# Kernel tuning notes

Measured on AMD Instinct MI355X. Metric: run time of the kernel, lower is better.

The kernel has to match this reference:

```python
import jax, jax.numpy as jnp
import numpy as np

N = 100000
E = 1600000
F_IN = 256
HID = 128
N_CLS = 2


def _glorot(k, shape):
    lim = float(np.sqrt(6.0 / (shape[0] + shape[1])))
    return jax.random.uniform(k, shape, jnp.float32, -lim, lim)


def setup_inputs() -> dict:
    key = jax.random.key(0)
    ks = jax.random.split(key, 10)
    x = jax.random.normal(ks[0], (N, F_IN), jnp.float32)
    edge_index = jax.random.randint(ks[1], (2, E), 0, N, dtype=jnp.int64)
    return {
        "x": x,
        "edge_index": edge_index,
        "W1": _glorot(ks[2], (F_IN, HID)), "b1": jnp.zeros((HID,), jnp.float32),
        "W2": _glorot(ks[3], (HID, HID)), "b2": jnp.zeros((HID,), jnp.float32),
        "W3": _glorot(ks[4], (HID, HID)), "b3": jnp.zeros((HID,), jnp.float32),
        "Wc": _glorot(ks[5], (HID, N_CLS)), "bc": jnp.zeros((N_CLS,), jnp.float32),
    }


def gcn_layer(x, W, b, src, dst, n):
    """PyG GCNConv: D^-1/2 (A+I) D^-1/2 X W + b with self-loops added."""
    xw = x @ W  # [N, H]
    # degree including the self-loop (all edge weights are 1)
    deg = jax.ops.segment_sum(jnp.ones((src.shape[0],), xw.dtype), dst,
                              num_segments=n) + 1.0
    dinv = jax.lax.rsqrt(deg)  # [N]
    norm = dinv[src] * dinv[dst]  # [E]
    msg = xw[src] * norm[:, None]  # [E, H] gathered+scaled messages
    out = jax.ops.segment_sum(msg, dst, num_segments=n)
    # self-loop contribution: norm = dinv[i]*dinv[i] = 1/deg[i]
    out = out + xw * (1.0 / deg)[:, None]
    return out + b


def reference(x, edge_index, W1, b1, W2, b2, W3, b3, Wc, bc):
    src, dst = edge_index[0], edge_index[1]
    h = jax.nn.relu(gcn_layer(x, W1, b1, src, dst, N))
    h = jax.nn.relu(gcn_layer(h, W2, b2, src, dst, N))  # dropout identity (eval)
    h = jax.nn.relu(gcn_layer(h, W3, b3, src, dst, N))
    logits = h @ Wc + bc  # [N, num_classes]
    return jax.nn.log_softmax(logits, axis=1)
```

## Files before the change

kernel.cpp:

```cpp
#include <hip/hip_runtime.h>
#include <hip/hip_bf16.h>
#include <cstdint>
#include <cstddef>

#define N_NODES 100000
#define N_EDGES 1600000
#define F_IN    256
#define HID     128
#define SCAN_BLK 1024
#define N_SCAN_BLOCKS ((N_NODES + SCAN_BLK - 1) / SCAN_BLK)
#define NB       ((N_NODES + 255) >> 8)
#define F3_CHUNK 7168
#define N_CHUNKS ((N_EDGES + F3_CHUNK - 1) / F3_CHUNK)

typedef __attribute__((ext_vector_type(8))) short  bf16x8;
typedef __attribute__((ext_vector_type(4))) float  f32x4;

static __device__ inline float bf2f(unsigned short u) {
    return __uint_as_float(((unsigned int)u) << 16);
}
static __device__ inline unsigned short f2bf(float f) {
    union { __hip_bfloat16 h; unsigned short u; } c;
    c.h = __float2bfloat16(f);
    return c.u;
}
static __device__ inline float lof(unsigned int w) { return __uint_as_float(w << 16); }
static __device__ inline float hif(unsigned int w) { return __uint_as_float(w & 0xffff0000u); }


__global__ __launch_bounds__(256) void zero_int_kernel(int* __restrict__ p, int n) {
    int i = blockIdx.x * 256 + threadIdx.x;
    if (i < n) p[i] = 0;
}
__global__ __launch_bounds__(256) void zero_f_kernel(float* __restrict__ p, int n) {
    int i = blockIdx.x * 256 + threadIdx.x;
    if (i < n) p[i] = 0.f;
}


__global__ __launch_bounds__(256) void bucket_count_kernel(const int* __restrict__ dst,
                                                           int* __restrict__ bcnt, int nE) {
    __shared__ int c[NB];
    for (int i = threadIdx.x; i < NB; i += 256) c[i] = 0;
    __syncthreads();
    int base = blockIdx.x * F3_CHUNK;
    int m = min(F3_CHUNK, nE - base);
    for (int t = threadIdx.x; t < m; t += 256)
        atomicAdd(&c[dst[base + t] >> 8], 1);
    __syncthreads();
    for (int i = threadIdx.x; i < NB; i += 256)
        if (c[i]) atomicAdd(&bcnt[i], c[i]);
}


__global__ __launch_bounds__(512) void scan_bucket_kernel(const int* __restrict__ bcnt,
                                                          int* __restrict__ bbase) {
    __shared__ int s[512];
    int t = threadIdx.x;
    int v = (t < NB) ? bcnt[t] : 0;
    s[t] = v;
    __syncthreads();
    for (int off = 1; off < 512; off <<= 1) {
        int add = (t >= off) ? s[t - off] : 0;
        __syncthreads();
        s[t] += add;
        __syncthreads();
    }
    if (t < NB) bbase[t] = s[t] - v;
    if (t == 0) bbase[NB] = N_EDGES;
}


__global__ __launch_bounds__(256) void stage_kernel(const int* __restrict__ src,
                                                    const int* __restrict__ dst,
                                                    const int* __restrict__ bbase,
                                                    int* __restrict__ gfill,
                                                    int* __restrict__ stg_src,
                                                    int* __restrict__ stg_dst, int nE) {
    __shared__ int ss[F3_CHUNK];
    __shared__ int sd[F3_CHUNK];
    __shared__ int cnt[NB];
    __shared__ int bas[NB];
    int base = blockIdx.x * F3_CHUNK;
    int m = min(F3_CHUNK, nE - base);
    for (int i = threadIdx.x; i < NB; i += 256) cnt[i] = 0;
    __syncthreads();
    for (int t = threadIdx.x; t < m; t += 256) {
        int s = src[base + t];
        int d = dst[base + t];
        ss[t] = s;
        sd[t] = d;
        atomicAdd(&cnt[d >> 8], 1);
    }
    __syncthreads();
    for (int i = threadIdx.x; i < NB; i += 256) {
        int c = cnt[i];
        bas[i] = bbase[i] + (c ? atomicAdd(&gfill[i], c) : 0);
        cnt[i] = 0;
    }
    __syncthreads();
    for (int t = threadIdx.x; t < m; t += 256) {
        int d = sd[t];
        int bkt = d >> 8;
        int k = atomicAdd(&cnt[bkt], 1);
        int pos = bas[bkt] + k;
        stg_src[pos] = ss[t];
        stg_dst[pos] = d;
    }
}


__global__ __launch_bounds__(256) void bucket_deg_kernel(const int* __restrict__ stg_dst,
                                                         const int* __restrict__ bbase,
                                                         int* __restrict__ deg, int n) {
    __shared__ int c[256];
    c[threadIdx.x] = 0;
    __syncthreads();
    int b = blockIdx.x;
    int beg = bbase[b], end = bbase[b + 1];
    for (int t = beg + threadIdx.x; t < end; t += 256)
        atomicAdd(&c[stg_dst[t] & 255], 1);
    __syncthreads();
    int node = b * 256 + threadIdx.x;
    if (node < n) deg[node] = c[threadIdx.x];
}


__global__ __launch_bounds__(256) void bucket_fill_kernel(const int* __restrict__ stg_src,
                                                          const int* __restrict__ stg_dst,
                                                          const int* __restrict__ bbase,
                                                          const int* __restrict__ row_ptr,
                                                          int* __restrict__ csr_src) {
    __shared__ int c[256];
    c[threadIdx.x] = 0;
    __syncthreads();
    int b = blockIdx.x;
    int beg = bbase[b], end = bbase[b + 1];
    for (int t = beg + threadIdx.x; t < end; t += 256) {
        int d = stg_dst[t];
        int k = atomicAdd(&c[d & 255], 1);
        csr_src[row_ptr[d] + k] = stg_src[t];
    }
}


__global__ __launch_bounds__(256) void dinv_kernel(const int* __restrict__ deg,
                                                   float* __restrict__ dinv, int n) {
    int i = blockIdx.x * 256 + threadIdx.x;
    if (i < n) dinv[i] = rsqrtf((float)deg[i] + 1.0f);
}


__global__ __launch_bounds__(256) void scan_reduce_kernel(const int* __restrict__ deg,
                                                          int n, int* __restrict__ blockSums) {
    __shared__ int red[256];
    int base = blockIdx.x * SCAN_BLK;
    int t = threadIdx.x;
    int s = 0;
#pragma unroll
    for (int k = 0; k < 4; ++k) {
        int idx = base + t * 4 + k;
        if (idx < n) s += deg[idx];
    }
    red[t] = s;
    __syncthreads();
    for (int off = 128; off > 0; off >>= 1) {
        if (t < off) red[t] += red[t + off];
        __syncthreads();
    }
    if (t == 0) blockSums[blockIdx.x] = red[0];
}

__global__ __launch_bounds__(128) void scan_small_kernel(int* __restrict__ data, int n) {
    __shared__ int s[128];
    int t = threadIdx.x;
    int v = (t < n) ? data[t] : 0;
    s[t] = v;
    __syncthreads();
    for (int off = 1; off < 128; off <<= 1) {
        int add = (t >= off) ? s[t - off] : 0;
        __syncthreads();
        s[t] += add;
        __syncthreads();
    }
    if (t < n) data[t] = s[t] - v;
}

__global__ __launch_bounds__(256) void scan_final_kernel(const int* __restrict__ deg, int n,
                                                         const int* __restrict__ blockSums,
                                                         int* __restrict__ row_ptr, int eTotal) {
    __shared__ int pre[256];
    int base = blockIdx.x * SCAN_BLK;
    int t = threadIdx.x;
    int v[4];
    int s = 0;
#pragma unroll
    for (int k = 0; k < 4; ++k) {
        int idx = base + t * 4 + k;
        v[k] = (idx < n) ? deg[idx] : 0;
        s += v[k];
    }
    pre[t] = s;
    __syncthreads();
    for (int off = 1; off < 256; off <<= 1) {
        int add = (t >= off) ? pre[t - off] : 0;
        __syncthreads();
        pre[t] += add;
        __syncthreads();
    }
    int running = blockSums[blockIdx.x] + pre[t] - s;
#pragma unroll
    for (int k = 0; k < 4; ++k) {
        int idx = base + t * 4 + k;
        if (idx < n) row_ptr[idx] = running;
        running += v[k];
    }
    if (blockIdx.x == 0 && t == 0) row_ptr[n] = eTotal;
}


template <int K>
__global__ __launch_bounds__(256) void prep_blob_kernel(const float* __restrict__ W,
                                                        unsigned short* __restrict__ blob) {
    constexpr int TOT = (K / 32) * 8 * 64;
    int tid = blockIdx.x * 256 + threadIdx.x;
    if (tid >= TOT) return;
    int lane = tid & 63;
    int c    = (tid >> 6) & 7;
    int s    = tid >> 9;
    int col  = c * 16 + (lane & 15);
    int kb   = s * 32 + (lane >> 4) * 8;
    bf16x8 o;
#pragma unroll
    for (int j = 0; j < 8; ++j)
        o[j] = (short)f2bf(W[(size_t)(kb + j) * HID + col]);
    *reinterpret_cast<bf16x8*>(blob + (size_t)tid * 8) = o;
}


template <int K, bool IN_BF16>
__global__ __launch_bounds__(256) void mfma_gemm_kernel(const void* __restrict__ Xv,
                                                        const unsigned short* __restrict__ blob,
                                                        unsigned short* __restrict__ Y, int n) {
    constexpr int KSTEPS = K / 32;
    const int lane = threadIdx.x & 63;
    const int wave = threadIdx.x >> 6;
    const int rowbase = blockIdx.x * 128 + wave * 32;

    const int r0 = min(rowbase +      (lane & 15), n - 1);
    const int r1 = min(rowbase + 16 + (lane & 15), n - 1);
    const int koff = (lane >> 4) * 8;

    f32x4 acc0[8], acc1[8];
#pragma unroll
    for (int c = 0; c < 8; ++c) { acc0[c] = (f32x4)0.f; acc1[c] = (f32x4)0.f; }

#pragma unroll
    for (int s = 0; s < KSTEPS; ++s) {
        bf16x8 bfr[8];
#pragma unroll
        for (int c = 0; c < 8; ++c)
            bfr[c] = *reinterpret_cast<const bf16x8*>(blob + ((size_t)((s * 8 + c) * 64 + lane)) * 8);

        bf16x8 a0, a1;
        if (IN_BF16) {
            const unsigned short* Xb = (const unsigned short*)Xv;
            a0 = *reinterpret_cast<const bf16x8*>(Xb + (size_t)r0 * K + s * 32 + koff);
            a1 = *reinterpret_cast<const bf16x8*>(Xb + (size_t)r1 * K + s * 32 + koff);
        } else {
            const float* Xf = (const float*)Xv;
            const float4* p0 = reinterpret_cast<const float4*>(Xf + (size_t)r0 * K + s * 32 + koff);
            const float4* p1 = reinterpret_cast<const float4*>(Xf + (size_t)r1 * K + s * 32 + koff);
            float4 q0 = p0[0], q1 = p0[1], q2 = p1[0], q3 = p1[1];
            a0[0] = (short)f2bf(q0.x); a0[1] = (short)f2bf(q0.y);
            a0[2] = (short)f2bf(q0.z); a0[3] = (short)f2bf(q0.w);
            a0[4] = (short)f2bf(q1.x); a0[5] = (short)f2bf(q1.y);
            a0[6] = (short)f2bf(q1.z); a0[7] = (short)f2bf(q1.w);
            a1[0] = (short)f2bf(q2.x); a1[1] = (short)f2bf(q2.y);
            a1[2] = (short)f2bf(q2.z); a1[3] = (short)f2bf(q2.w);
            a1[4] = (short)f2bf(q3.x); a1[5] = (short)f2bf(q3.y);
            a1[6] = (short)f2bf(q3.z); a1[7] = (short)f2bf(q3.w);
        }

#pragma unroll
        for (int c = 0; c < 8; ++c) {
            acc0[c] = __builtin_amdgcn_mfma_f32_16x16x32_bf16(a0, bfr[c], acc0[c], 0, 0, 0);
            acc1[c] = __builtin_amdgcn_mfma_f32_16x16x32_bf16(a1, bfr[c], acc1[c], 0, 0, 0);
        }
    }

    const int col  = lane & 15;
    const int rsub = (lane >> 4) * 4;
#pragma unroll
    for (int c = 0; c < 8; ++c) {
#pragma unroll
        for (int r = 0; r < 4; ++r) {
            int row0 = rowbase + rsub + r;
            int row1 = rowbase + 16 + rsub + r;
            if (row0 < n) Y[(size_t)row0 * HID + c * 16 + col] = f2bf(acc0[c][r]);
            if (row1 < n) Y[(size_t)row1 * HID + c * 16 + col] = f2bf(acc1[c][r]);
        }
    }
}


__global__ __launch_bounds__(256) void agg_gather_kernel(const unsigned short* __restrict__ xw,
                                                         const float* __restrict__ dinv,
                                                         const int* __restrict__ row_ptr,
                                                         const int* __restrict__ csr_src,
                                                         const float* __restrict__ b,
                                                         unsigned short* __restrict__ h, int n) {
    int v = (blockIdx.x * 256 + threadIdx.x) >> 6;
    if (v >= n) return;
    int lane = threadIdx.x & 63;

    int beg = __builtin_amdgcn_readfirstlane(row_ptr[v]);
    int end = __builtin_amdgcn_readfirstlane(row_ptr[v + 1]);

    const unsigned int* xw32 = (const unsigned int*)xw;
    float a0 = 0.f, a1 = 0.f;

    int j = beg;
    for (; j + 4 <= end; j += 4) {
        int s0 = __builtin_amdgcn_readfirstlane(csr_src[j + 0]);
        int s1 = __builtin_amdgcn_readfirstlane(csr_src[j + 1]);
        int s2 = __builtin_amdgcn_readfirstlane(csr_src[j + 2]);
        int s3 = __builtin_amdgcn_readfirstlane(csr_src[j + 3]);
        float d0 = dinv[s0], d1 = dinv[s1], d2 = dinv[s2], d3 = dinv[s3];
        unsigned int w0 = xw32[(size_t)s0 * 64 + lane];
        unsigned int w1 = xw32[(size_t)s1 * 64 + lane];
        unsigned int w2 = xw32[(size_t)s2 * 64 + lane];
        unsigned int w3 = xw32[(size_t)s3 * 64 + lane];
        a0 = fmaf(d0, lof(w0), a0); a1 = fmaf(d0, hif(w0), a1);
        a0 = fmaf(d1, lof(w1), a0); a1 = fmaf(d1, hif(w1), a1);
        a0 = fmaf(d2, lof(w2), a0); a1 = fmaf(d2, hif(w2), a1);
        a0 = fmaf(d3, lof(w3), a0); a1 = fmaf(d3, hif(w3), a1);
    }
    for (; j < end; ++j) {
        int s0 = __builtin_amdgcn_readfirstlane(csr_src[j]);
        float d0 = dinv[s0];
        unsigned int w0 = xw32[(size_t)s0 * 64 + lane];
        a0 = fmaf(d0, lof(w0), a0); a1 = fmaf(d0, hif(w0), a1);
    }

    float dv = dinv[v];
    unsigned int wv = xw32[(size_t)v * 64 + lane];
    float2 bb = *reinterpret_cast<const float2*>(b + 2 * lane);
    float s2v = dv * dv;
    float r0 = fmaxf(dv * a0 + s2v * lof(wv) + bb.x, 0.f);
    float r1 = fmaxf(dv * a1 + s2v * hif(wv) + bb.y, 0.f);
    ushort2 o;
    o.x = f2bf(r0);
    o.y = f2bf(r1);
    *reinterpret_cast<ushort2*>(h + (size_t)v * HID + 2 * lane) = o;
}


__global__ __launch_bounds__(256) void classifier_kernel(const unsigned short* __restrict__ h,
                                                         const float* __restrict__ Wc,
                                                         const float* __restrict__ bc,
                                                         float* __restrict__ out, int n) {
    __shared__ float wc0[HID], wc1[HID], bcs[2];
    if (threadIdx.x < HID) {
        wc0[threadIdx.x] = Wc[threadIdx.x * 2 + 0];
        wc1[threadIdx.x] = Wc[threadIdx.x * 2 + 1];
    }
    if (threadIdx.x < 2) bcs[threadIdx.x] = bc[threadIdx.x];
    __syncthreads();

    int i = blockIdx.x * 256 + threadIdx.x;
    if (i >= n) return;
    const ushort4* hr = reinterpret_cast<const ushort4*>(h + (size_t)i * HID);
    float l0 = 0.f, l1 = 0.f;
#pragma unroll
    for (int j4 = 0; j4 < 32; ++j4) {
        ushort4 q = hr[j4];
        float v0 = bf2f(q.x), v1 = bf2f(q.y), v2 = bf2f(q.z), v3 = bf2f(q.w);
        l0 += v0 * wc0[j4 * 4 + 0] + v1 * wc0[j4 * 4 + 1]
            + v2 * wc0[j4 * 4 + 2] + v3 * wc0[j4 * 4 + 3];
        l1 += v0 * wc1[j4 * 4 + 0] + v1 * wc1[j4 * 4 + 1]
            + v2 * wc1[j4 * 4 + 2] + v3 * wc1[j4 * 4 + 3];
    }
    l0 += bcs[0]; l1 += bcs[1];
    float m = fmaxf(l0, l1);
    float lse = m + logf(expf(l0 - m) + expf(l1 - m));
    out[i * 2 + 0] = l0 - lse;
    out[i * 2 + 1] = l1 - lse;
}


static inline size_t align256(size_t x) { return (x + 255) & ~(size_t)255; }

extern "C" void kernel_launch(void* const* d_in, const int* in_sizes, int n_in,
                              void* d_out, int out_size, void* d_ws, size_t ws_size,
                              hipStream_t stream) {
    const float* x   = (const float*)d_in[0];
    const int*   ei  = (const int*)d_in[1];
    const float* W1  = (const float*)d_in[2];
    const float* b1  = (const float*)d_in[3];
    const float* W2  = (const float*)d_in[4];
    const float* b2  = (const float*)d_in[5];
    const float* W3  = (const float*)d_in[6];
    const float* b3  = (const float*)d_in[7];
    const float* Wc  = (const float*)d_in[8];
    const float* bc  = (const float*)d_in[9];
    float*       out = (float*)d_out;

    const int* src = ei;
    const int* dst = ei + N_EDGES;

    size_t off = 0;
    size_t o_dinv    = off; off = align256(off + (size_t)N_NODES * 4);
    size_t o_deg     = off; off = align256(off + (size_t)N_NODES * 4);
    size_t o_rowptr  = off; off = align256(off + (size_t)(N_NODES + 1) * 4);
    size_t o_bsums   = off; off = align256(off + (size_t)N_SCAN_BLOCKS * 4);
    size_t o_bcnt    = off; off = align256(off + (size_t)NB * 4);
    size_t o_bbase   = off; off = align256(off + (size_t)(NB + 1) * 4);
    size_t o_gfill   = off; off = align256(off + (size_t)NB * 4);
    size_t o_csr     = off; off = align256(off + (size_t)N_EDGES * 4);
    size_t o_stgs    = off; off = align256(off + (size_t)N_EDGES * 4);
    size_t o_stgd    = off; off = align256(off + (size_t)N_EDGES * 4);
    size_t o_blob1   = off; off = align256(off + (size_t)(F_IN / 32) * 8 * 64 * 8 * 2);
    size_t o_blob2   = off; off = align256(off + (size_t)(HID / 32) * 8 * 64 * 8 * 2);
    size_t o_blob3   = off; off = align256(off + (size_t)(HID / 32) * 8 * 64 * 8 * 2);
    size_t o_bufA    = off; off = align256(off + (size_t)N_NODES * HID * 2);
    size_t o_bufB    = off; off = align256(off + (size_t)N_NODES * HID * 2);
    size_t need = off;

    const int nThr = 256;
    const int gOut = (out_size + nThr - 1) / nThr;
    if (ws_size < need) {
        zero_f_kernel<<<gOut, nThr, 0, stream>>>(out, out_size);
        return;
    }

    char* ws = (char*)d_ws;
    float*          dinv    = (float*)(ws + o_dinv);
    int*            deg     = (int*)(ws + o_deg);
    int*            row_ptr = (int*)(ws + o_rowptr);
    int*            bsums   = (int*)(ws + o_bsums);
    int*            bcnt    = (int*)(ws + o_bcnt);
    int*            bbase   = (int*)(ws + o_bbase);
    int*            gfill   = (int*)(ws + o_gfill);
    int*            csr_src = (int*)(ws + o_csr);
    int*            stg_src = (int*)(ws + o_stgs);
    int*            stg_dst = (int*)(ws + o_stgd);
    unsigned short* blob1   = (unsigned short*)(ws + o_blob1);
    unsigned short* blob2   = (unsigned short*)(ws + o_blob2);
    unsigned short* blob3   = (unsigned short*)(ws + o_blob3);
    unsigned short* bufA    = (unsigned short*)(ws + o_bufA);
    unsigned short* bufB    = (unsigned short*)(ws + o_bufB);

    const int gN = (N_NODES + nThr - 1) / nThr;
    const int gW = (N_NODES * 64 + nThr - 1) / nThr;
    const int gG = (N_NODES + 127) / 128;

    zero_int_kernel<<<(NB + 255) / 256, nThr, 0, stream>>>(bcnt, NB);
    zero_int_kernel<<<(NB + 255) / 256, nThr, 0, stream>>>(gfill, NB);
    bucket_count_kernel<<<N_CHUNKS, nThr, 0, stream>>>(dst, bcnt, N_EDGES);
    scan_bucket_kernel<<<1, 512, 0, stream>>>(bcnt, bbase);
    stage_kernel<<<N_CHUNKS, nThr, 0, stream>>>(src, dst, bbase, gfill,
                                                stg_src, stg_dst, N_EDGES);
    bucket_deg_kernel<<<NB, nThr, 0, stream>>>(stg_dst, bbase, deg, N_NODES);
    dinv_kernel<<<gN, nThr, 0, stream>>>(deg, dinv, N_NODES);
    scan_reduce_kernel<<<N_SCAN_BLOCKS, nThr, 0, stream>>>(deg, N_NODES, bsums);
    scan_small_kernel<<<1, 128, 0, stream>>>(bsums, N_SCAN_BLOCKS);
    scan_final_kernel<<<N_SCAN_BLOCKS, nThr, 0, stream>>>(deg, N_NODES, bsums, row_ptr, N_EDGES);
    bucket_fill_kernel<<<NB, nThr, 0, stream>>>(stg_src, stg_dst, bbase, row_ptr, csr_src);

    prep_blob_kernel<F_IN><<<16, nThr, 0, stream>>>(W1, blob1);
    prep_blob_kernel<HID><<<8, nThr, 0, stream>>>(W2, blob2);
    prep_blob_kernel<HID><<<8, nThr, 0, stream>>>(W3, blob3);

    mfma_gemm_kernel<F_IN, false><<<gG, nThr, 0, stream>>>(x, blob1, bufA, N_NODES);
    agg_gather_kernel<<<gW, nThr, 0, stream>>>(bufA, dinv, row_ptr, csr_src, b1, bufB, N_NODES);

    mfma_gemm_kernel<HID, true><<<gG, nThr, 0, stream>>>(bufB, blob2, bufA, N_NODES);
    agg_gather_kernel<<<gW, nThr, 0, stream>>>(bufA, dinv, row_ptr, csr_src, b2, bufB, N_NODES);

    mfma_gemm_kernel<HID, true><<<gG, nThr, 0, stream>>>(bufB, blob3, bufA, N_NODES);
    agg_gather_kernel<<<gW, nThr, 0, stream>>>(bufA, dinv, row_ptr, csr_src, b3, bufB, N_NODES);

    classifier_kernel<<<gN, nThr, 0, stream>>>(bufB, Wc, bc, out, N_NODES);
}
```

Measured before the change: 361.6 us.

## Pack staged edges, fuse classifier into last aggregation, add nontemporal hints

Staged edges are packed into one 32-bit word (source shifted left by 8 bits with the destination's low 8 bits), which halves staging traffic and removes the source array from the stage kernel's shared memory. The final aggregation is templated so that it computes the classifier logits and log-softmax with a wave reduction, which removes the write and re-read of the last hidden layer and one kernel launch. Nontemporal loads and stores are added on streaming accesses, and the two zeroing launches are merged into one by placing the two count arrays next to each other. Packing relies on source ids fitting in 24 bits, and the nontemporal hints could hurt reuse of data in the cache.

Result: slower. 407.3 us (+12.7%).

```diff
diff --git a/kernel.cpp b/kernel.cpp
--- a/kernel.cpp
+++ b/kernel.cpp
@@ -46,12 +46,11 @@
     int base = blockIdx.x * F3_CHUNK;
     int m = min(F3_CHUNK, nE - base);
     for (int t = threadIdx.x; t < m; t += 256)
-        atomicAdd(&c[dst[base + t] >> 8], 1);
+        atomicAdd(&c[__builtin_nontemporal_load(&dst[base + t]) >> 8], 1);
     __syncthreads();
     for (int i = threadIdx.x; i < NB; i += 256)
         if (c[i]) atomicAdd(&bcnt[i], c[i]);
 }
-
 
 __global__ __launch_bounds__(512) void scan_bucket_kernel(const int* __restrict__ bcnt,
                                                           int* __restrict__ bbase) {
@@ -75,9 +74,7 @@
                                                     const int* __restrict__ dst,
                                                     const int* __restrict__ bbase,
                                                     int* __restrict__ gfill,
-                                                    int* __restrict__ stg_src,
-                                                    int* __restrict__ stg_dst, int nE) {
-    __shared__ int ss[F3_CHUNK];
+                                                    unsigned int* __restrict__ stg, int nE) {
     __shared__ int sd[F3_CHUNK];
     __shared__ int cnt[NB];
     __shared__ int bas[NB];
@@ -86,9 +83,7 @@
     for (int i = threadIdx.x; i < NB; i += 256) cnt[i] = 0;
     __syncthreads();
     for (int t = threadIdx.x; t < m; t += 256) {
-        int s = src[base + t];
-        int d = dst[base + t];
-        ss[t] = s;
+        int d = __builtin_nontemporal_load(&dst[base + t]);
         sd[t] = d;
         atomicAdd(&cnt[d >> 8], 1);
     }
@@ -102,15 +97,14 @@
     for (int t = threadIdx.x; t < m; t += 256) {
         int d = sd[t];
         int bkt = d >> 8;
+        int s = __builtin_nontemporal_load(&src[base + t]);
         int k = atomicAdd(&cnt[bkt], 1);
-        int pos = bas[bkt] + k;
-        stg_src[pos] = ss[t];
-        stg_dst[pos] = d;
-    }
-}
-
-
-__global__ __launch_bounds__(256) void bucket_deg_kernel(const int* __restrict__ stg_dst,
+        __builtin_nontemporal_store(((unsigned int)s << 8) | (unsigned int)(d & 255),
+                                    &stg[bas[bkt] + k]);
+    }
+}
+
+__global__ __launch_bounds__(256) void bucket_deg_kernel(const unsigned int* __restrict__ stg,
                                                          const int* __restrict__ bbase,
                                                          int* __restrict__ deg, int n) {
     __shared__ int c[256];
@@ -119,15 +113,13 @@
     int b = blockIdx.x;
     int beg = bbase[b], end = bbase[b + 1];
     for (int t = beg + threadIdx.x; t < end; t += 256)
-        atomicAdd(&c[stg_dst[t] & 255], 1);
+        atomicAdd(&c[__builtin_nontemporal_load(&stg[t]) & 255u], 1);
     __syncthreads();
     int node = b * 256 + threadIdx.x;
     if (node < n) deg[node] = c[threadIdx.x];
 }
 
-
-__global__ __launch_bounds__(256) void bucket_fill_kernel(const int* __restrict__ stg_src,
-                                                          const int* __restrict__ stg_dst,
+__global__ __launch_bounds__(256) void bucket_fill_kernel(const unsigned int* __restrict__ stg,
                                                           const int* __restrict__ bbase,
                                                           const int* __restrict__ row_ptr,
                                                           int* __restrict__ csr_src) {
@@ -137,9 +129,12 @@
     int b = blockIdx.x;
     int beg = bbase[b], end = bbase[b + 1];
     for (int t = beg + threadIdx.x; t < end; t += 256) {
-        int d = stg_dst[t];
-        int k = atomicAdd(&c[d & 255], 1);
-        csr_src[row_ptr[d] + k] = stg_src[t];
+        unsigned int p = __builtin_nontemporal_load(&stg[t]);
+        int dl = (int)(p & 255u);
+        int s  = (int)(p >> 8);
+        int k = atomicAdd(&c[dl], 1);
+        int d = b * 256 + dl;
+        csr_src[row_ptr[d] + k] = s;
     }
 }
 
@@ -304,28 +299,32 @@
 }
 
 
+template <bool CLS>
 __global__ __launch_bounds__(256) void agg_gather_kernel(const unsigned short* __restrict__ xw,
                                                          const float* __restrict__ dinv,
                                                          const int* __restrict__ row_ptr,
                                                          const int* __restrict__ csr_src,
                                                          const float* __restrict__ b,
-                                                         unsigned short* __restrict__ h, int n) {
+                                                         unsigned short* __restrict__ h,
+                                                         const float* __restrict__ Wc,
+                                                         const float* __restrict__ bc,
+                                                         float* __restrict__ out, int n) {
     int v = (blockIdx.x * 256 + threadIdx.x) >> 6;
     if (v >= n) return;
     int lane = threadIdx.x & 63;
 
-    int beg = __builtin_amdgcn_readfirstlane(row_ptr[v]);
-    int end = __builtin_amdgcn_readfirstlane(row_ptr[v + 1]);
+    int beg = __builtin_amdgcn_readfirstlane(__builtin_nontemporal_load(&row_ptr[v]));
+    int end = __builtin_amdgcn_readfirstlane(__builtin_nontemporal_load(&row_ptr[v + 1]));
 
     const unsigned int* xw32 = (const unsigned int*)xw;
     float a0 = 0.f, a1 = 0.f;
 
     int j = beg;
     for (; j + 4 <= end; j += 4) {
-        int s0 = __builtin_amdgcn_readfirstlane(csr_src[j + 0]);
-        int s1 = __builtin_amdgcn_readfirstlane(csr_src[j + 1]);
-        int s2 = __builtin_amdgcn_readfirstlane(csr_src[j + 2]);
-        int s3 = __builtin_amdgcn_readfirstlane(csr_src[j + 3]);
+        int s0 = __builtin_amdgcn_readfirstlane(__builtin_nontemporal_load(&csr_src[j + 0]));
+        int s1 = __builtin_amdgcn_readfirstlane(__builtin_nontemporal_load(&csr_src[j + 1]));
+        int s2 = __builtin_amdgcn_readfirstlane(__builtin_nontemporal_load(&csr_src[j + 2]));
+        int s3 = __builtin_amdgcn_readfirstlane(__builtin_nontemporal_load(&csr_src[j + 3]));
         float d0 = dinv[s0], d1 = dinv[s1], d2 = dinv[s2], d3 = dinv[s3];
         unsigned int w0 = xw32[(size_t)s0 * 64 + lane];
         unsigned int w1 = xw32[(size_t)s1 * 64 + lane];
@@ -337,7 +336,7 @@
         a0 = fmaf(d3, lof(w3), a0); a1 = fmaf(d3, hif(w3), a1);
     }
     for (; j < end; ++j) {
-        int s0 = __builtin_amdgcn_readfirstlane(csr_src[j]);
+        int s0 = __builtin_amdgcn_readfirstlane(__builtin_nontemporal_load(&csr_src[j]));
         float d0 = dinv[s0];
         unsigned int w0 = xw32[(size_t)s0 * 64 + lane];
         a0 = fmaf(d0, lof(w0), a0); a1 = fmaf(d0, hif(w0), a1);
@@ -349,43 +348,29 @@
     float s2v = dv * dv;
     float r0 = fmaxf(dv * a0 + s2v * lof(wv) + bb.x, 0.f);
     float r1 = fmaxf(dv * a1 + s2v * hif(wv) + bb.y, 0.f);
-    ushort2 o;
-    o.x = f2bf(r0);
-    o.y = f2bf(r1);
-    *reinterpret_cast<ushort2*>(h + (size_t)v * HID + 2 * lane) = o;
-}
-
-
-__global__ __launch_bounds__(256) void classifier_kernel(const unsigned short* __restrict__ h,
-                                                         const float* __restrict__ Wc,
-                                                         const float* __restrict__ bc,
-                                                         float* __restrict__ out, int n) {
-    __shared__ float wc0[HID], wc1[HID], bcs[2];
-    if (threadIdx.x < HID) {
-        wc0[threadIdx.x] = Wc[threadIdx.x * 2 + 0];
-        wc1[threadIdx.x] = Wc[threadIdx.x * 2 + 1];
-    }
-    if (threadIdx.x < 2) bcs[threadIdx.x] = bc[threadIdx.x];
-    __syncthreads();
-
-    int i = blockIdx.x * 256 + threadIdx.x;
-    if (i >= n) return;
-    const ushort4* hr = reinterpret_cast<const ushort4*>(h + (size_t)i * HID);
-    float l0 = 0.f, l1 = 0.f;
-#pragma unroll
-    for (int j4 = 0; j4 < 32; ++j4) {
-        ushort4 q = hr[j4];
-        float v0 = bf2f(q.x), v1 = bf2f(q.y), v2 = bf2f(q.z), v3 = bf2f(q.w);
-        l0 += v0 * wc0[j4 * 4 + 0] + v1 * wc0[j4 * 4 + 1]
-            + v2 * wc0[j4 * 4 + 2] + v3 * wc0[j4 * 4 + 3];
-        l1 += v0 * wc1[j4 * 4 + 0] + v1 * wc1[j4 * 4 + 1]
-            + v2 * wc1[j4 * 4 + 2] + v3 * wc1[j4 * 4 + 3];
-    }
-    l0 += bcs[0]; l1 += bcs[1];
-    float m = fmaxf(l0, l1);
-    float lse = m + logf(expf(l0 - m) + expf(l1 - m));
-    out[i * 2 + 0] = l0 - lse;
-    out[i * 2 + 1] = l1 - lse;
+
+    if (!CLS) {
+        unsigned int o = (unsigned int)f2bf(r0) | ((unsigned int)f2bf(r1) << 16);
+        __builtin_nontemporal_store(o,
+            reinterpret_cast<unsigned int*>(h + (size_t)v * HID + 2 * lane));
+    } else {
+        float4 qw = *reinterpret_cast<const float4*>(Wc + 4 * lane);
+        float p0 = r0 * qw.x + r1 * qw.z;
+        float p1 = r0 * qw.y + r1 * qw.w;
+#pragma unroll
+        for (int off = 1; off < 64; off <<= 1) {
+            p0 += __shfl_xor(p0, off);
+            p1 += __shfl_xor(p1, off);
+        }
+        if (lane == 0) {
+            float l0 = p0 + bc[0];
+            float l1 = p1 + bc[1];
+            float m = fmaxf(l0, l1);
+            float lse = m + logf(expf(l0 - m) + expf(l1 - m));
+            out[(size_t)v * 2 + 0] = l0 - lse;
+            out[(size_t)v * 2 + 1] = l1 - lse;
+        }
+    }
 }
 
 
@@ -414,12 +399,12 @@
     size_t o_deg     = off; off = align256(off + (size_t)N_NODES * 4);
     size_t o_rowptr  = off; off = align256(off + (size_t)(N_NODES + 1) * 4);
     size_t o_bsums   = off; off = align256(off + (size_t)N_SCAN_BLOCKS * 4);
-    size_t o_bcnt    = off; off = align256(off + (size_t)NB * 4);
+    size_t o_bcnt    = off;
+    size_t o_gfill   = o_bcnt + (size_t)NB * 4;
+                            off = align256(o_gfill + (size_t)NB * 4);
     size_t o_bbase   = off; off = align256(off + (size_t)(NB + 1) * 4);
-    size_t o_gfill   = off; off = align256(off + (size_t)NB * 4);
     size_t o_csr     = off; off = align256(off + (size_t)N_EDGES * 4);
-    size_t o_stgs    = off; off = align256(off + (size_t)N_EDGES * 4);
-    size_t o_stgd    = off; off = align256(off + (size_t)N_EDGES * 4);
+    size_t o_stg     = off; off = align256(off + (size_t)N_EDGES * 4);
     size_t o_blob1   = off; off = align256(off + (size_t)(F_IN / 32) * 8 * 64 * 8 * 2);
     size_t o_blob2   = off; off = align256(off + (size_t)(HID / 32) * 8 * 64 * 8 * 2);
     size_t o_blob3   = off; off = align256(off + (size_t)(HID / 32) * 8 * 64 * 8 * 2);
@@ -440,11 +425,10 @@
     int*            row_ptr = (int*)(ws + o_rowptr);
     int*            bsums   = (int*)(ws + o_bsums);
     int*            bcnt    = (int*)(ws + o_bcnt);
+    int*            gfill   = (int*)(ws + o_gfill);
     int*            bbase   = (int*)(ws + o_bbase);
-    int*            gfill   = (int*)(ws + o_gfill);
     int*            csr_src = (int*)(ws + o_csr);
-    int*            stg_src = (int*)(ws + o_stgs);
-    int*            stg_dst = (int*)(ws + o_stgd);
+    unsigned int*   stg     = (unsigned int*)(ws + o_stg);
     unsigned short* blob1   = (unsigned short*)(ws + o_blob1);
     unsigned short* blob2   = (unsigned short*)(ws + o_blob2);
     unsigned short* blob3   = (unsigned short*)(ws + o_blob3);
@@ -455,31 +439,30 @@
     const int gW = (N_NODES * 64 + nThr - 1) / nThr;
     const int gG = (N_NODES + 127) / 128;
 
-    zero_int_kernel<<<(NB + 255) / 256, nThr, 0, stream>>>(bcnt, NB);
-    zero_int_kernel<<<(NB + 255) / 256, nThr, 0, stream>>>(gfill, NB);
+    zero_int_kernel<<<(2 * NB + 255) / 256, nThr, 0, stream>>>(bcnt, 2 * NB);
     bucket_count_kernel<<<N_CHUNKS, nThr, 0, stream>>>(dst, bcnt, N_EDGES);
     scan_bucket_kernel<<<1, 512, 0, stream>>>(bcnt, bbase);
-    stage_kernel<<<N_CHUNKS, nThr, 0, stream>>>(src, dst, bbase, gfill,
-                                                stg_src, stg_dst, N_EDGES);
-    bucket_deg_kernel<<<NB, nThr, 0, stream>>>(stg_dst, bbase, deg, N_NODES);
+    stage_kernel<<<N_CHUNKS, nThr, 0, stream>>>(src, dst, bbase, gfill, stg, N_EDGES);
+    bucket_deg_kernel<<<NB, nThr, 0, stream>>>(stg, bbase, deg, N_NODES);
     dinv_kernel<<<gN, nThr, 0, stream>>>(deg, dinv, N_NODES);
     scan_reduce_kernel<<<N_SCAN_BLOCKS, nThr, 0, stream>>>(deg, N_NODES, bsums);
     scan_small_kernel<<<1, 128, 0, stream>>>(bsums, N_SCAN_BLOCKS);
     scan_final_kernel<<<N_SCAN_BLOCKS, nThr, 0, stream>>>(deg, N_NODES, bsums, row_ptr, N_EDGES);
-    bucket_fill_kernel<<<NB, nThr, 0, stream>>>(stg_src, stg_dst, bbase, row_ptr, csr_src);
+    bucket_fill_kernel<<<NB, nThr, 0, stream>>>(stg, bbase, row_ptr, csr_src);
 
     prep_blob_kernel<F_IN><<<16, nThr, 0, stream>>>(W1, blob1);
     prep_blob_kernel<HID><<<8, nThr, 0, stream>>>(W2, blob2);
     prep_blob_kernel<HID><<<8, nThr, 0, stream>>>(W3, blob3);
 
     mfma_gemm_kernel<F_IN, false><<<gG, nThr, 0, stream>>>(x, blob1, bufA, N_NODES);
-    agg_gather_kernel<<<gW, nThr, 0, stream>>>(bufA, dinv, row_ptr, csr_src, b1, bufB, N_NODES);
+    agg_gather_kernel<false><<<gW, nThr, 0, stream>>>(bufA, dinv, row_ptr, csr_src, b1,
+                                                      bufB, nullptr, nullptr, nullptr, N_NODES);
 
     mfma_gemm_kernel<HID, true><<<gG, nThr, 0, stream>>>(bufB, blob2, bufA, N_NODES);
-    agg_gather_kernel<<<gW, nThr, 0, stream>>>(bufA, dinv, row_ptr, csr_src, b2, bufB, N_NODES);
+    agg_gather_kernel<false><<<gW, nThr, 0, stream>>>(bufA, dinv, row_ptr, csr_src, b2,
+                                                      bufB, nullptr, nullptr, nullptr, N_NODES);
 
     mfma_gemm_kernel<HID, true><<<gG, nThr, 0, stream>>>(bufB, blob3, bufA, N_NODES);
-    agg_gather_kernel<<<gW, nThr, 0, stream>>>(bufA, dinv, row_ptr, csr_src, b3, bufB, N_NODES);
-
-    classifier_kernel<<<gN, nThr, 0, stream>>>(bufB, Wc, bc, out, N_NODES);
-}
+    agg_gather_kernel<true><<<gW, nThr, 0, stream>>>(bufA, dinv, row_ptr, csr_src, b3,
+                                                     nullptr, Wc, bc, out, N_NODES);
+}
```
